# Kernel optimization log

Hardware: AMD Instinct MI355X
Metric: run time of the kernel (lower is better)

The kernel has to match this reference:

```python
import jax, jax.numpy as jnp
import numpy as np

D_MODEL = 2048
N_HEADS = 16
KV_GROUPS = 4
D_K = D_MODEL // N_HEADS  # 128


def setup_inputs() -> dict:
    key = jax.random.key(0)
    ks = jax.random.split(key, 9)
    B, S = 2, 2048
    scale = 0.02
    return {
        "x": jax.random.normal(ks[0], (B, S, D_MODEL), dtype=jnp.float32),
        "Wq": jax.random.normal(ks[1], (D_MODEL, D_MODEL), dtype=jnp.float32) * scale,
        "bq": jnp.zeros((D_MODEL,), dtype=jnp.float32),
        "Wk": jax.random.normal(ks[2], (D_MODEL, KV_GROUPS * D_K), dtype=jnp.float32) * scale,
        "bk": jnp.zeros((KV_GROUPS * D_K,), dtype=jnp.float32),
        "Wv": jax.random.normal(ks[3], (D_MODEL, KV_GROUPS * D_K), dtype=jnp.float32) * scale,
        "bv": jnp.zeros((KV_GROUPS * D_K,), dtype=jnp.float32),
        "Wo": jax.random.normal(ks[4], (D_MODEL, D_MODEL), dtype=jnp.float32) * scale,
        "bo": jnp.zeros((D_MODEL,), dtype=jnp.float32),
    }


def reference(x, Wq, bq, Wk, bk, Wv, bv, Wo, bo):
    B, S, _ = x.shape
    rep = N_HEADS // KV_GROUPS
    # Projections
    Q = (x @ Wq + bq).reshape(B, S, N_HEADS, D_K)      # [B,S,H,Dk]
    K = (x @ Wk + bk).reshape(B, S, KV_GROUPS, D_K)    # [B,S,G,Dk]
    V = (x @ Wv + bv).reshape(B, S, KV_GROUPS, D_K)
    # Group queries: [B,S,G,rep,Dk] so each group of rep heads shares one KV head
    Qg = Q.reshape(B, S, KV_GROUPS, rep, D_K)
    # scores: [B,G,rep,S_q,S_k]
    scores = jnp.einsum('bsgrd,btgd->bgrst', Qg, K) / jnp.sqrt(jnp.asarray(D_K, x.dtype))
    attn = jax.nn.softmax(scores, axis=-1)
    out = jnp.einsum('bgrst,btgd->bsgrd', attn, V)     # [B,S,G,rep,Dk]
    out = out.reshape(B, S, D_MODEL)
    return out @ Wo + bo
```

## Files before the change

### kernel.cpp

```cpp
#include <hip/hip_runtime.h>
#include <math.h>
#include <stdint.h>

#define D_MODEL 2048
#define SS 2048
#define BB 2
#define ROWS (BB*SS)
#define NQKV 3072

typedef __attribute__((ext_vector_type(8))) short bf16x8;
typedef __attribute__((ext_vector_type(4))) float f32x4;
typedef __attribute__((ext_vector_type(16))) float f32x16;
typedef __attribute__((ext_vector_type(4))) unsigned int u32x4;
typedef __attribute__((ext_vector_type(8))) unsigned short ushort8v;
typedef __attribute__((ext_vector_type(4))) unsigned short ushort4v;

#define KSCALE 0.12751879566649053f

__device__ __forceinline__ unsigned short f2bf(float f) {
  uint32_t u = __builtin_bit_cast(uint32_t, f);
  return (unsigned short)((u + 0x7FFFu + ((u >> 16) & 1u)) >> 16);
}

#define MFMA16x16x32 __builtin_amdgcn_mfma_f32_16x16x32_bf16
#define MFMA32x32x16 __builtin_amdgcn_mfma_f32_32x32x16_bf16

#define GLOAD16(gsrc, ldst) \
  __builtin_amdgcn_global_load_lds((const __attribute__((address_space(1))) void*)(gsrc), \
      (__attribute__((address_space(3))) void*)(ldst), 16, 0, 0)

__global__ __launch_bounds__(256)
void conv_x(const float* __restrict__ x, unsigned short* __restrict__ xb) {
  size_t i = ((size_t)blockIdx.x * 256 + threadIdx.x) * 8;
  float4 v0 = *(const float4*)(x + i);
  float4 v1 = *(const float4*)(x + i + 4);
  ushort8v o;
  o[0]=f2bf(v0.x); o[1]=f2bf(v0.y); o[2]=f2bf(v0.z); o[3]=f2bf(v0.w);
  o[4]=f2bf(v1.x); o[5]=f2bf(v1.y); o[6]=f2bf(v1.z); o[7]=f2bf(v1.w);
  *(ushort8v*)(xb + i) = o;
}

__global__ __launch_bounds__(256)
void pack_wqkvT(const float* __restrict__ Wq, const float* __restrict__ Wk,
                const float* __restrict__ Wv, unsigned short* __restrict__ WT) {
  __shared__ float T[32][33];
  const int k0 = blockIdx.x * 32, n0 = blockIdx.y * 32;
  const int tid = threadIdx.x;
  const float* W; int nbase, stride; float fac = 1.0f;
  if (n0 < 2048)      { W = Wq; nbase = n0;        stride = 2048; }
  else if (n0 < 2560) { W = Wk; nbase = n0 - 2048; stride = 512; fac = KSCALE; }
  else                { W = Wv; nbase = n0 - 2560; stride = 512;  }
  int r = tid >> 3, c = (tid & 7) * 4;
  float4 v = *(const float4*)(W + (size_t)(k0 + r) * stride + nbase + c);
  T[c + 0][r] = v.x; T[c + 1][r] = v.y; T[c + 2][r] = v.z; T[c + 3][r] = v.w;
  __syncthreads();
  ushort4v o;
  o[0]=f2bf(T[r][c]*fac); o[1]=f2bf(T[r][c+1]*fac);
  o[2]=f2bf(T[r][c+2]*fac); o[3]=f2bf(T[r][c+3]*fac);
  *(ushort4v*)(WT + (size_t)(n0 + r) * 2048 + k0 + c) = o;
}

__global__ __launch_bounds__(256)
void pack_woT(const float* __restrict__ Wo, unsigned short* __restrict__ WoT) {
  __shared__ float T[32][33];
  const int k0 = blockIdx.x * 32, n0 = blockIdx.y * 32;
  const int tid = threadIdx.x;
  int r = tid >> 3, c = (tid & 7) * 4;
  float4 v = *(const float4*)(Wo + (size_t)(k0 + r) * 2048 + n0 + c);
  T[c+0][r]=v.x; T[c+1][r]=v.y; T[c+2][r]=v.z; T[c+3][r]=v.w;
  __syncthreads();
  ushort4v o;
#pragma unroll
  for (int j = 0; j < 4; ++j) o[j] = f2bf(T[r][c + j]);
  *(ushort4v*)(WoT + (size_t)(n0 + r) * 2048 + k0 + c) = o;
}

__global__ void pack_bias(const float* __restrict__ bq, const float* __restrict__ bk,
                          const float* __restrict__ bv, float* __restrict__ bqkv) {
  int i = blockIdx.x * 256 + threadIdx.x;
  if (i >= 3072) return;
  bqkv[i] = i < 2048 ? bq[i]
          : (i < 2560 ? bk[i - 2048] * KSCALE : bv[i - 2560]);
}

__global__ __launch_bounds__(256)
void gemm_qkv(const unsigned short* __restrict__ A,
              const unsigned short* __restrict__ BT,
              const float* __restrict__ bias,
              unsigned short* __restrict__ Cv,
              unsigned short* __restrict__ VTp) {
  __shared__ unsigned short As[128 * 64];
  __shared__ unsigned short Bs[128 * 64];
  const int tid = threadIdx.x;
  const int w = tid >> 6, l = tid & 63;
  const int bm = blockIdx.y * 128, bn = blockIdx.x * 128;
  const int mbase = (w & 1) * 64, nbase = (w >> 1) * 64;

  f32x4 acc[4][4] = {};

  for (int t = 0; t < 32; ++t) {
    const int k = t * 64;
    __syncthreads();
#pragma unroll
    for (int i = 0; i < 4; ++i) {
      int r0 = w * 32 + i * 8;
      int row = r0 + (l >> 3);
      int gr = l & 7;
      GLOAD16(A + (size_t)(bm + row) * 2048 + k + ((gr ^ (row & 7)) << 3), As + r0 * 64);
      GLOAD16(BT + (size_t)(bn + row) * 2048 + k + ((gr ^ (row & 7)) << 3), Bs + r0 * 64);
    }
    __syncthreads();
#pragma unroll
    for (int ks = 0; ks < 2; ++ks) {
      bf16x8 af[4], bfr[4];
#pragma unroll
      for (int mb = 0; mb < 4; ++mb) {
        int row = mbase + mb * 16 + (l & 15);
        int g = ks * 4 + (l >> 4);
        af[mb] = *(const bf16x8*)((const char*)As + row * 128 + ((g ^ (row & 7)) << 4));
      }
#pragma unroll
      for (int nb = 0; nb < 4; ++nb) {
        int row = nbase + nb * 16 + (l & 15);
        int g = ks * 4 + (l >> 4);
        bfr[nb] = *(const bf16x8*)((const char*)Bs + row * 128 + ((g ^ (row & 7)) << 4));
      }
#pragma unroll
      for (int mb = 0; mb < 4; ++mb)
#pragma unroll
        for (int nb = 0; nb < 4; ++nb)
          acc[mb][nb] = MFMA16x16x32(af[mb], bfr[nb], acc[mb][nb], 0, 0, 0);
    }
  }

  if (bn >= 2560) {
#pragma unroll
    for (int mb = 0; mb < 4; ++mb) {
      int row0 = bm + mbase + mb * 16 + (l >> 4) * 4;
      int bidx = row0 >> 11, tok = row0 & 2047;
#pragma unroll
      for (int nb = 0; nb < 4; ++nb) {
        int col = bn + nbase + nb * 16 + (l & 15);
        ushort4v o;
#pragma unroll
        for (int r = 0; r < 4; ++r) o[r] = f2bf(acc[mb][nb][r] + bias[col]);
        *(ushort4v*)(VTp + ((size_t)(bidx * 512 + col - 2560)) * 2048 + tok) = o;
      }
    }
    return;
  }
#pragma unroll
  for (int mb = 0; mb < 4; ++mb) {
#pragma unroll
    for (int nb = 0; nb < 4; ++nb) {
#pragma unroll
      for (int r = 0; r < 4; ++r) {
        int row = bm + mbase + mb * 16 + (l >> 4) * 4 + r;
        int col = bn + nbase + nb * 16 + (l & 15);
        Cv[(size_t)row * NQKV + col] = f2bf(acc[mb][nb][r] + bias[col]);
      }
    }
  }
}

__global__ __launch_bounds__(256)
void gemm_out(const unsigned short* __restrict__ A,
              const unsigned short* __restrict__ BT,
              const float* __restrict__ bias,
              float* __restrict__ C) {
  __shared__ unsigned short As[128 * 64];
  __shared__ unsigned short Bs[128 * 64];
  const int tid = threadIdx.x;
  const int w = tid >> 6, l = tid & 63;
  const int bm = blockIdx.y * 128, bn = blockIdx.x * 128;
  const int mbase = (w & 1) * 64, nbase = (w >> 1) * 64;

  f32x4 acc[4][4] = {};

  for (int t = 0; t < 32; ++t) {
    const int k = t * 64;
    __syncthreads();
#pragma unroll
    for (int i = 0; i < 4; ++i) {
      int r0 = w * 32 + i * 8;
      int row = r0 + (l >> 3);
      int gr = l & 7;
      GLOAD16(A + (size_t)(bm + row) * 2048 + k + ((gr ^ (row & 7)) << 3), As + r0 * 64);
      GLOAD16(BT + (size_t)(bn + row) * 2048 + k + ((gr ^ (row & 7)) << 3), Bs + r0 * 64);
    }
    __syncthreads();
#pragma unroll
    for (int ks = 0; ks < 2; ++ks) {
      bf16x8 af[4], bfr[4];
#pragma unroll
      for (int mb = 0; mb < 4; ++mb) {
        int row = mbase + mb * 16 + (l & 15);
        int g = ks * 4 + (l >> 4);
        af[mb] = *(const bf16x8*)((const char*)As + row * 128 + ((g ^ (row & 7)) << 4));
      }
#pragma unroll
      for (int nb = 0; nb < 4; ++nb) {
        int row = nbase + nb * 16 + (l & 15);
        int g = ks * 4 + (l >> 4);
        bfr[nb] = *(const bf16x8*)((const char*)Bs + row * 128 + ((g ^ (row & 7)) << 4));
      }
#pragma unroll
      for (int mb = 0; mb < 4; ++mb)
#pragma unroll
        for (int nb = 0; nb < 4; ++nb)
          acc[mb][nb] = MFMA16x16x32(af[mb], bfr[nb], acc[mb][nb], 0, 0, 0);
    }
  }

#pragma unroll
  for (int mb = 0; mb < 4; ++mb) {
#pragma unroll
    for (int nb = 0; nb < 4; ++nb) {
#pragma unroll
      for (int r = 0; r < 4; ++r) {
        int row = bm + mbase + mb * 16 + (l >> 4) * 4 + r;
        int col = bn + nbase + nb * 16 + (l & 15);
        C[(size_t)row * 2048 + col] = acc[mb][nb][r] + bias[col];
      }
    }
  }
}

__global__ __launch_bounds__(256, 2)
void attn_mfma(const unsigned short* __restrict__ QKV,
               const unsigned short* __restrict__ VT,
               unsigned short* __restrict__ AOp) {
  __shared__ unsigned short Ks[2][64 * 128];
  __shared__ unsigned short VsT[2][128 * 64];
  const int tid = threadIdx.x;
  const int w = tid >> 6, l = tid & 63;
  const int qt = blockIdx.x;
  const int bh = blockIdx.y;
  const int b = bh >> 4, hh = bh & 15, g = hh >> 2;
  const int h = l >> 5;
  const int q = l & 31;

  bf16x8 qf[8];
  {
    const int qrow = b * SS + qt * 128 + w * 32 + q;
    const unsigned short* qp = QKV + (size_t)qrow * NQKV + hh * 128 + h * 8;
#pragma unroll
    for (int kk = 0; kk < 8; ++kk) qf[kk] = *(const bf16x8*)(qp + kk * 16);
  }

  f32x16 oaccT[4] = {};
  float mrow = -1e30f, lrow = 0.f;

  const unsigned short* kbase = QKV + (size_t)b * SS * NQKV + 2048 + g * 128;
  const unsigned short* vtbase = VT + (size_t)(b * 4 + g) * 128 * 2048;

#define STAGE_KV(buf, ktile) do { \
    _Pragma("unroll") \
    for (int i = 0; i < 4; ++i) { \
      int r0 = w * 16 + i * 4; \
      int row = r0 + (l >> 4); \
      int gr = l & 15; \
      GLOAD16(kbase + (size_t)((ktile) * 64 + row) * NQKV + ((gr ^ (row & 15)) << 3), \
              &Ks[buf][r0 * 128]); \
    } \
    _Pragma("unroll") \
    for (int i = 0; i < 4; ++i) { \
      int r0 = w * 32 + i * 8; \
      int row = r0 + (l >> 3); \
      int gr = l & 7; \
      GLOAD16(vtbase + (size_t)row * 2048 + (ktile) * 64 + ((gr ^ (row & 7)) << 3), \
              &VsT[buf][r0 * 64]); \
    } \
  } while (0)

  STAGE_KV(0, 0);
  int cur = 0;

  for (int kt = 0; kt < SS / 64; ++kt) {
    if (kt + 1 < SS / 64) {
      STAGE_KV(cur ^ 1, kt + 1);
      asm volatile("s_waitcnt vmcnt(8)" ::: "memory");
    } else {
      asm volatile("s_waitcnt vmcnt(0)" ::: "memory");
    }
    __builtin_amdgcn_s_barrier();

    const unsigned short* Kc = Ks[cur];
    const unsigned short* Vc = VsT[cur];

    f32x16 sacc[2] = {};
    __builtin_amdgcn_s_setprio(1);
#pragma unroll
    for (int kk = 0; kk < 8; ++kk) {
#pragma unroll
      for (int kb = 0; kb < 2; ++kb) {
        int key = kb * 32 + q;
        bf16x8 kf = *(const bf16x8*)((const char*)Kc + key * 256
                                     + (((kk * 2 + h) ^ (key & 15)) << 4));
        sacc[kb] = MFMA32x32x16(kf, qf[kk], sacc[kb], 0, 0, 0);
      }
    }
    __builtin_amdgcn_s_setprio(0);

    float pmax = sacc[0][0];
#pragma unroll
    for (int r = 1; r < 16; ++r) pmax = fmaxf(pmax, sacc[0][r]);
#pragma unroll
    for (int r = 0; r < 16; ++r) pmax = fmaxf(pmax, sacc[1][r]);
    pmax = fmaxf(pmax, __shfl_xor(pmax, 32, 64));
    if (__any(pmax > mrow + 11.5416f)) {
      float mnew = fmaxf(mrow, pmax);
      float alpha = __builtin_amdgcn_exp2f(mrow - mnew);
      lrow *= alpha;
      mrow = mnew;
#pragma unroll
      for (int db = 0; db < 4; ++db)
#pragma unroll
        for (int r = 0; r < 16; ++r) oaccT[db][r] *= alpha;
    }
    float e[2][16];
    float ssum = 0.f;
#pragma unroll
    for (int kb = 0; kb < 2; ++kb)
#pragma unroll
      for (int r = 0; r < 16; ++r) {
        e[kb][r] = __builtin_amdgcn_exp2f(sacc[kb][r] - mrow);
        ssum += e[kb][r];
      }
    ssum += __shfl_xor(ssum, 32, 64);
    lrow += ssum;

    bf16x8 pf[4];
#pragma unroll
    for (int ks = 0; ks < 4; ++ks) {
      const int kb = ks >> 1, r0 = (ks & 1) * 8;
      uint32_t w0, w1, w2, w3;
      asm("v_cvt_pk_bf16_f32 %0, %1, %2" : "=v"(w0) : "v"(e[kb][r0+0]), "v"(e[kb][r0+1]));
      asm("v_cvt_pk_bf16_f32 %0, %1, %2" : "=v"(w1) : "v"(e[kb][r0+2]), "v"(e[kb][r0+3]));
      asm("v_cvt_pk_bf16_f32 %0, %1, %2" : "=v"(w2) : "v"(e[kb][r0+4]), "v"(e[kb][r0+5]));
      asm("v_cvt_pk_bf16_f32 %0, %1, %2" : "=v"(w3) : "v"(e[kb][r0+6]), "v"(e[kb][r0+7]));
      uint32_t s1 = h ? w0 : w2;
      uint32_t s2 = h ? w1 : w3;
      uint32_t r1 = __shfl_xor((int)s1, 32, 64);
      uint32_t r2 = __shfl_xor((int)s2, 32, 64);
      u32x4 u;
      u[0] = h ? r1 : w0;
      u[1] = h ? r2 : w1;
      u[2] = h ? w2 : r1;
      u[3] = h ? w3 : r2;
      pf[ks] = __builtin_bit_cast(bf16x8, u);
    }

    __builtin_amdgcn_s_setprio(1);
#pragma unroll
    for (int ks = 0; ks < 4; ++ks) {
#pragma unroll
      for (int db = 0; db < 4; ++db) {
        int d = db * 32 + q;
        bf16x8 vf = *(const bf16x8*)((const char*)Vc + d * 128
                                     + (((ks * 2 + h) ^ (d & 7)) << 4));
        oaccT[db] = MFMA32x32x16(vf, pf[ks], oaccT[db], 0, 0, 0);
      }
    }
    __builtin_amdgcn_s_setprio(0);

    __builtin_amdgcn_s_barrier();
    cur ^= 1;
  }
#undef STAGE_KV

  float rl = 1.0f / lrow;
  char* lbase = (char*)Ks + w * 8192;
#pragma unroll
  for (int db = 0; db < 4; ++db) {
#pragma unroll
    for (int r = 0; r < 16; r += 2) {
      float f0 = oaccT[db][r] * rl, f1 = oaccT[db][r + 1] * rl;
      uint32_t pk2;
      asm("v_cvt_pk_bf16_f32 %0, %1, %2" : "=v"(pk2) : "v"(f0), "v"(f1));
      int slot = db * 4 + (r >> 2);
      int phys = slot ^ q;
      phys = (slot ^ (q & 15));
      *(uint32_t*)(lbase + q * 256 + phys * 16 + 8 * h + 2 * (r & 3)) = pk2;
    }
  }
#pragma unroll
  for (int i = 0; i < 8; ++i) {
    int row = i * 4 + (l >> 4);
    int slot = l & 15;
    int phys = slot ^ (row & 15);
    u32x4 vv = *(const u32x4*)(lbase + row * 256 + phys * 16);
    *(u32x4*)(AOp + (size_t)(b * SS + qt * 128 + w * 32 + row) * 2048
              + hh * 128 + slot * 8) = vv;
  }
}

extern "C" void kernel_launch(void* const* d_in, const int* in_sizes, int n_in,
                              void* d_out, int out_size, void* d_ws, size_t ws_size,
                              hipStream_t stream) {
  const float* x  = (const float*)d_in[0];
  const float* Wq = (const float*)d_in[1];
  const float* bq = (const float*)d_in[2];
  const float* Wk = (const float*)d_in[3];
  const float* bk = (const float*)d_in[4];
  const float* Wv = (const float*)d_in[5];
  const float* bv = (const float*)d_in[6];
  const float* Wo = (const float*)d_in[7];
  const float* bo = (const float*)d_in[8];
  float* out = (float*)d_out;

  char* ws = (char*)d_ws;
  unsigned short* x_bf  = (unsigned short*)(ws);
  unsigned short* WqkvT = (unsigned short*)(ws + 16777216);
  unsigned short* AO    = (unsigned short*)(ws);
  float*          bqkv  = (float*)(ws + 35651584);
  unsigned short* WoT   = (unsigned short*)(ws + 36700160);
  unsigned short* QKV   = (unsigned short*)(ws + 54525952);
  unsigned short* VT    = (unsigned short*)(ws + 79691776);

  conv_x<<<4096, 256, 0, stream>>>(x, x_bf);
  pack_wqkvT<<<dim3(64, 96), 256, 0, stream>>>(Wq, Wk, Wv, WqkvT);
  pack_bias<<<12, 256, 0, stream>>>(bq, bk, bv, bqkv);
  pack_woT<<<dim3(64, 64), 256, 0, stream>>>(Wo, WoT);
  gemm_qkv<<<dim3(24, 32), 256, 0, stream>>>(x_bf, WqkvT, bqkv, QKV, VT);
  attn_mfma<<<dim3(16, 32), 256, 0, stream>>>(QKV, VT, AO);
  gemm_out<<<dim3(16, 32), 256, 0, stream>>>(AO, WoT, bo, out);
}
```

Before: 225.8 us.

## Process two query sub-blocks per wave in attention to reuse K/V fragments

```diff
diff --git a/kernel.cpp b/kernel.cpp
--- a/kernel.cpp
+++ b/kernel.cpp
@@ -226,12 +226,11 @@
   }
 }
 
-__global__ __launch_bounds__(256, 2)
+__global__ __launch_bounds__(256, 1)
 void attn_mfma(const unsigned short* __restrict__ QKV,
                const unsigned short* __restrict__ VT,
                unsigned short* __restrict__ AOp) {
-  __shared__ unsigned short Ks[2][64 * 128];
-  __shared__ unsigned short VsT[2][128 * 64];
+  __shared__ unsigned short SB[32768];
   const int tid = threadIdx.x;
   const int w = tid >> 6, l = tid & 63;
   const int qt = blockIdx.x;
@@ -240,16 +239,18 @@
   const int h = l >> 5;
   const int q = l & 31;
 
-  bf16x8 qf[8];
-  {
-    const int qrow = b * SS + qt * 128 + w * 32 + q;
+  bf16x8 qf[2][8];
+#pragma unroll
+  for (int qb = 0; qb < 2; ++qb) {
+    const int qrow = b * SS + qt * 256 + w * 64 + qb * 32 + q;
     const unsigned short* qp = QKV + (size_t)qrow * NQKV + hh * 128 + h * 8;
 #pragma unroll
-    for (int kk = 0; kk < 8; ++kk) qf[kk] = *(const bf16x8*)(qp + kk * 16);
-  }
-
-  f32x16 oaccT[4] = {};
-  float mrow = -1e30f, lrow = 0.f;
+    for (int kk = 0; kk < 8; ++kk) qf[qb][kk] = *(const bf16x8*)(qp + kk * 16);
+  }
+
+  f32x16 oaccT[4][2] = {};
+  float mrow[2] = {-1e30f, -1e30f};
+  float lrow[2] = {0.f, 0.f};
 
   const unsigned short* kbase = QKV + (size_t)b * SS * NQKV + 2048 + g * 128;
   const unsigned short* vtbase = VT + (size_t)(b * 4 + g) * 128 * 2048;
@@ -261,7 +262,7 @@
       int row = r0 + (l >> 4); \
       int gr = l & 15; \
       GLOAD16(kbase + (size_t)((ktile) * 64 + row) * NQKV + ((gr ^ (row & 15)) << 3), \
-              &Ks[buf][r0 * 128]); \
+              SB + (buf) * 8192 + r0 * 128); \
     } \
     _Pragma("unroll") \
     for (int i = 0; i < 4; ++i) { \
@@ -269,7 +270,7 @@
       int row = r0 + (l >> 3); \
       int gr = l & 7; \
       GLOAD16(vtbase + (size_t)row * 2048 + (ktile) * 64 + ((gr ^ (row & 7)) << 3), \
-              &VsT[buf][r0 * 64]); \
+              SB + 16384 + (buf) * 8192 + r0 * 64); \
     } \
   } while (0)
 
@@ -285,10 +286,10 @@
     }
     __builtin_amdgcn_s_barrier();
 
-    const unsigned short* Kc = Ks[cur];
-    const unsigned short* Vc = VsT[cur];
-
-    f32x16 sacc[2] = {};
+    const unsigned short* Kc = SB + cur * 8192;
+    const unsigned short* Vc = SB + 16384 + cur * 8192;
+
+    f32x16 sacc[2][2] = {};
     __builtin_amdgcn_s_setprio(1);
 #pragma unroll
     for (int kk = 0; kk < 8; ++kk) {
@@ -297,58 +298,70 @@
         int key = kb * 32 + q;
         bf16x8 kf = *(const bf16x8*)((const char*)Kc + key * 256
                                      + (((kk * 2 + h) ^ (key & 15)) << 4));
-        sacc[kb] = MFMA32x32x16(kf, qf[kk], sacc[kb], 0, 0, 0);
+#pragma unroll
+        for (int qb = 0; qb < 2; ++qb)
+          sacc[kb][qb] = MFMA32x32x16(kf, qf[qb][kk], sacc[kb][qb], 0, 0, 0);
       }
     }
     __builtin_amdgcn_s_setprio(0);
 
-    float pmax = sacc[0][0];
-#pragma unroll
-    for (int r = 1; r < 16; ++r) pmax = fmaxf(pmax, sacc[0][r]);
-#pragma unroll
-    for (int r = 0; r < 16; ++r) pmax = fmaxf(pmax, sacc[1][r]);
-    pmax = fmaxf(pmax, __shfl_xor(pmax, 32, 64));
-    if (__any(pmax > mrow + 11.5416f)) {
-      float mnew = fmaxf(mrow, pmax);
-      float alpha = __builtin_amdgcn_exp2f(mrow - mnew);
-      lrow *= alpha;
-      mrow = mnew;
-#pragma unroll
-      for (int db = 0; db < 4; ++db)
-#pragma unroll
-        for (int r = 0; r < 16; ++r) oaccT[db][r] *= alpha;
-    }
-    float e[2][16];
-    float ssum = 0.f;
-#pragma unroll
-    for (int kb = 0; kb < 2; ++kb)
-#pragma unroll
-      for (int r = 0; r < 16; ++r) {
-        e[kb][r] = __builtin_amdgcn_exp2f(sacc[kb][r] - mrow);
-        ssum += e[kb][r];
-      }
-    ssum += __shfl_xor(ssum, 32, 64);
-    lrow += ssum;
-
-    bf16x8 pf[4];
-#pragma unroll
-    for (int ks = 0; ks < 4; ++ks) {
-      const int kb = ks >> 1, r0 = (ks & 1) * 8;
-      uint32_t w0, w1, w2, w3;
-      asm("v_cvt_pk_bf16_f32 %0, %1, %2" : "=v"(w0) : "v"(e[kb][r0+0]), "v"(e[kb][r0+1]));
-      asm("v_cvt_pk_bf16_f32 %0, %1, %2" : "=v"(w1) : "v"(e[kb][r0+2]), "v"(e[kb][r0+3]));
-      asm("v_cvt_pk_bf16_f32 %0, %1, %2" : "=v"(w2) : "v"(e[kb][r0+4]), "v"(e[kb][r0+5]));
-      asm("v_cvt_pk_bf16_f32 %0, %1, %2" : "=v"(w3) : "v"(e[kb][r0+6]), "v"(e[kb][r0+7]));
-      uint32_t s1 = h ? w0 : w2;
-      uint32_t s2 = h ? w1 : w3;
-      uint32_t r1 = __shfl_xor((int)s1, 32, 64);
-      uint32_t r2 = __shfl_xor((int)s2, 32, 64);
-      u32x4 u;
-      u[0] = h ? r1 : w0;
-      u[1] = h ? r2 : w1;
-      u[2] = h ? w2 : r1;
-      u[3] = h ? w3 : r2;
-      pf[ks] = __builtin_bit_cast(bf16x8, u);
+#pragma unroll
+    for (int qb = 0; qb < 2; ++qb) {
+      float pmax = sacc[0][qb][0];
+#pragma unroll
+      for (int r = 1; r < 16; ++r) pmax = fmaxf(pmax, sacc[0][qb][r]);
+#pragma unroll
+      for (int r = 0; r < 16; ++r) pmax = fmaxf(pmax, sacc[1][qb][r]);
+      pmax = fmaxf(pmax, __shfl_xor(pmax, 32, 64));
+      if (__any(pmax > mrow[qb] + 11.5416f)) {
+        float mnew = fmaxf(mrow[qb], pmax);
+        float alpha = __builtin_amdgcn_exp2f(mrow[qb] - mnew);
+        lrow[qb] *= alpha;
+        mrow[qb] = mnew;
+#pragma unroll
+        for (int db = 0; db < 4; ++db)
+#pragma unroll
+          for (int r = 0; r < 16; ++r) oaccT[db][qb][r] *= alpha;
+      }
+      float ssum = 0.f;
+#pragma unroll
+      for (int kb = 0; kb < 2; ++kb)
+#pragma unroll
+        for (int r = 0; r < 16; ++r) {
+          float e = __builtin_amdgcn_exp2f(sacc[kb][qb][r] - mrow[qb]);
+          sacc[kb][qb][r] = e;
+          ssum += e;
+        }
+      ssum += __shfl_xor(ssum, 32, 64);
+      lrow[qb] += ssum;
+    }
+
+    bf16x8 pf[2][4];
+#pragma unroll
+    for (int qb = 0; qb < 2; ++qb) {
+#pragma unroll
+      for (int ks = 0; ks < 4; ++ks) {
+        const int kb = ks >> 1, r0 = (ks & 1) * 8;
+        uint32_t w0, w1, w2, w3;
+        asm("v_cvt_pk_bf16_f32 %0, %1, %2" : "=v"(w0)
+            : "v"(sacc[kb][qb][r0+0]), "v"(sacc[kb][qb][r0+1]));
+        asm("v_cvt_pk_bf16_f32 %0, %1, %2" : "=v"(w1)
+            : "v"(sacc[kb][qb][r0+2]), "v"(sacc[kb][qb][r0+3]));
+        asm("v_cvt_pk_bf16_f32 %0, %1, %2" : "=v"(w2)
+            : "v"(sacc[kb][qb][r0+4]), "v"(sacc[kb][qb][r0+5]));
+        asm("v_cvt_pk_bf16_f32 %0, %1, %2" : "=v"(w3)
+            : "v"(sacc[kb][qb][r0+6]), "v"(sacc[kb][qb][r0+7]));
+        uint32_t s1 = h ? w0 : w2;
+        uint32_t s2 = h ? w1 : w3;
+        uint32_t r1 = __shfl_xor((int)s1, 32, 64);
+        uint32_t r2 = __shfl_xor((int)s2, 32, 64);
+        u32x4 u;
+        u[0] = h ? r1 : w0;
+        u[1] = h ? r2 : w1;
+        u[2] = h ? w2 : r1;
+        u[3] = h ? w3 : r2;
+        pf[qb][ks] = __builtin_bit_cast(bf16x8, u);
+      }
     }
 
     __builtin_amdgcn_s_setprio(1);
@@ -359,7 +372,9 @@
         int d = db * 32 + q;
         bf16x8 vf = *(const bf16x8*)((const char*)Vc + d * 128
                                      + (((ks * 2 + h) ^ (d & 7)) << 4));
-        oaccT[db] = MFMA32x32x16(vf, pf[ks], oaccT[db], 0, 0, 0);
+#pragma unroll
+        for (int qb = 0; qb < 2; ++qb)
+          oaccT[db][qb] = MFMA32x32x16(vf, pf[qb][ks], oaccT[db][qb], 0, 0, 0);
       }
     }
     __builtin_amdgcn_s_setprio(0);
@@ -369,28 +384,33 @@
   }
 #undef STAGE_KV
 
-  float rl = 1.0f / lrow;
-  char* lbase = (char*)Ks + w * 8192;
-#pragma unroll
-  for (int db = 0; db < 4; ++db) {
-#pragma unroll
-    for (int r = 0; r < 16; r += 2) {
-      float f0 = oaccT[db][r] * rl, f1 = oaccT[db][r + 1] * rl;
-      uint32_t pk2;
-      asm("v_cvt_pk_bf16_f32 %0, %1, %2" : "=v"(pk2) : "v"(f0), "v"(f1));
-      int slot = db * 4 + (r >> 2);
-      int phys = slot ^ q;
-      phys = (slot ^ (q & 15));
-      *(uint32_t*)(lbase + q * 256 + phys * 16 + 8 * h + 2 * (r & 3)) = pk2;
-    }
-  }
-#pragma unroll
-  for (int i = 0; i < 8; ++i) {
+  __syncthreads();
+  char* lbase = (char*)SB + w * 16384;
+#pragma unroll
+  for (int qb = 0; qb < 2; ++qb) {
+    float rl = 1.0f / lrow[qb];
+    int row = qb * 32 + q;
+#pragma unroll
+    for (int db = 0; db < 4; ++db) {
+#pragma unroll
+      for (int r = 0; r < 16; r += 2) {
+        float f0 = oaccT[db][qb][r] * rl, f1 = oaccT[db][qb][r + 1] * rl;
+        uint32_t pk2;
+        asm("v_cvt_pk_bf16_f32 %0, %1, %2" : "=v"(pk2) : "v"(f0), "v"(f1));
+        int slot = db * 4 + (r >> 2);
+        int phys = slot ^ (row & 15);
+        *(uint32_t*)(lbase + row * 256 + phys * 16 + ((r & 3) << 1) + (h << 3)) = pk2;
+      }
+    }
+  }
+  __syncthreads();
+#pragma unroll
+  for (int i = 0; i < 16; ++i) {
     int row = i * 4 + (l >> 4);
     int slot = l & 15;
     int phys = slot ^ (row & 15);
     u32x4 vv = *(const u32x4*)(lbase + row * 256 + phys * 16);
-    *(u32x4*)(AOp + (size_t)(b * SS + qt * 128 + w * 32 + row) * 2048
+    *(u32x4*)(AOp + (size_t)(b * SS + qt * 256 + w * 64 + row) * 2048
               + hh * 128 + slot * 8) = vv;
   }
 }
@@ -423,6 +443,6 @@
   pack_bias<<<12, 256, 0, stream>>>(bq, bk, bv, bqkv);
   pack_woT<<<dim3(64, 64), 256, 0, stream>>>(Wo, WoT);
   gemm_qkv<<<dim3(24, 32), 256, 0, stream>>>(x_bf, WqkvT, bqkv, QKV, VT);
-  attn_mfma<<<dim3(16, 32), 256, 0, stream>>>(QKV, VT, AO);
+  attn_mfma<<<dim3(8, 32), 256, 0, stream>>>(QKV, VT, AO);
   gemm_out<<<dim3(16, 32), 256, 0, stream>>>(AO, WoT, bo, out);
 }
```

New measurement: 241.7 us. +7.1%, slower.
